# Kernel optimization log

Measured on AMD Instinct MI355X. Metric: run time of the kernel, lower is better.

Reference implementation:

```python
import jax, jax.numpy as jnp
import numpy as np

EPS = 1e-5  # BatchNorm eps


def _conv3x3(x, w, b):
    # x: [B,C,H,W], w: [O,C,3,3], b: [O]
    y = jax.lax.conv_general_dilated(
        x, w, window_strides=(1, 1), padding=((1, 1), (1, 1)),
        dimension_numbers=("NCHW", "OIHW", "NCHW"))
    return y + b[None, :, None, None]


def _bilinear_gather(x, py, px):
    """Bilinear sample x at fractional coords (zero outside bounds).
    x: [B,C,H,W]; py, px: [B,K,H,W] -> returns [B,C,K,H,W]."""
    B, C, H, W = x.shape
    K = py.shape[1]
    x_flat = x.reshape(B, C, H * W)
    y0 = jnp.floor(py)
    x0 = jnp.floor(px)
    wy1 = py - y0
    wx1 = px - x0
    wy0 = 1.0 - wy1
    wx0 = 1.0 - wx1

    def gather(yi, xi):
        valid = (yi >= 0) & (yi <= H - 1) & (xi >= 0) & (xi <= W - 1)
        yc = jnp.clip(yi, 0, H - 1).astype(jnp.int32)
        xc = jnp.clip(xi, 0, W - 1).astype(jnp.int32)
        idx = (yc * W + xc).reshape(B, 1, K * H * W)
        g = jnp.take_along_axis(x_flat, idx, axis=2).reshape(B, C, K, H, W)
        return g * valid.astype(x.dtype)[:, None]

    val = (gather(y0, x0) * (wy0 * wx0)[:, None]
           + gather(y0, x0 + 1.0) * (wy0 * wx1)[:, None]
           + gather(y0 + 1.0, x0) * (wy1 * wx0)[:, None]
           + gather(y0 + 1.0, x0 + 1.0) * (wy1 * wx1)[:, None])
    return val


def _deform_conv_bn_relu(x, w_off, b_off, w_dcn, b_dcn, gamma, beta):
    B, Ci, H, W = x.shape
    Co = w_dcn.shape[0]
    # offset/mask branch: 27 = 9 dy | 9 dx (cat, then interpreted interleaved) | 9 mask
    om = _conv3x3(x, w_off, b_off)                       # [B,27,H,W]
    offset = jnp.concatenate([om[:, :9], om[:, 9:18]], axis=1)  # [B,18,H,W]
    mask = jax.nn.sigmoid(om[:, 18:27])                  # [B,9,H,W]
    dy = offset[:, 0::2]                                 # [B,9,H,W]
    dx = offset[:, 1::2]                                 # [B,9,H,W]
    # base sampling grid: stride 1, pad 1, dilation 1, 3x3 kernel
    ky = jnp.repeat(jnp.arange(3, dtype=x.dtype), 3)     # [9]
    kx = jnp.tile(jnp.arange(3, dtype=x.dtype), 3)       # [9]
    hh = jnp.arange(H, dtype=x.dtype)
    ww = jnp.arange(W, dtype=x.dtype)
    py = dy + (hh - 1.0)[None, None, :, None] + ky[None, :, None, None]
    px = dx + (ww - 1.0)[None, None, None, :] + kx[None, :, None, None]
    sampled = _bilinear_gather(x, py, px)                # [B,Ci,9,H,W]
    sampled = sampled * mask[:, None]                    # modulated (DCNv2)
    out = jnp.einsum('bckhw,ock->bohw', sampled, w_dcn.reshape(Co, Ci, 9))
    out = out + b_dcn[None, :, None, None]
    # BatchNorm2d (training mode: batch statistics, biased variance) + ReLU
    mean = jnp.mean(out, axis=(0, 2, 3), keepdims=True)
    var = jnp.mean(jnp.square(out - mean), axis=(0, 2, 3), keepdims=True)
    bn = (out - mean) * jax.lax.rsqrt(var + EPS)
    bn = bn * gamma[None, :, None, None] + beta[None, :, None, None]
    return jax.nn.relu(bn)


def setup_inputs() -> dict:
    key = jax.random.key(0)
    k0, k1, k2 = jax.random.split(key, 3)
    B, Ci, Co, H, W = 2, 256, 256, 96, 96
    x = jax.random.normal(k0, (B, Ci, H, W), jnp.float32)
    # small offset-conv weights -> offsets within a few pixels (realistic after training)
    w_off = jax.random.normal(k1, (27, Ci, 3, 3), jnp.float32) * 0.01
    b_off = jnp.zeros((27,), jnp.float32)
    w_dcn = jax.random.normal(k2, (Co, Ci, 3, 3), jnp.float32) * (1.0 / np.sqrt(Ci * 9))
    b_dcn = jnp.zeros((Co,), jnp.float32)
    gamma = jnp.ones((Co,), jnp.float32)
    beta = jnp.zeros((Co,), jnp.float32)
    return {"x": x, "w_off": w_off, "b_off": b_off, "w_dcn": w_dcn,
            "b_dcn": b_dcn, "gamma": gamma, "beta": beta}


def reference(x, w_off, b_off, w_dcn, b_dcn, gamma, beta):
    return _deform_conv_bn_relu(x, w_off, b_off, w_dcn, b_dcn, gamma, beta)
```

## Files before the change

kernel.cpp:

```cpp
#include <hip/hip_runtime.h>


typedef unsigned short ushort_t;
typedef unsigned int uint_t;
typedef __attribute__((ext_vector_type(8))) short bf16x8;
typedef __attribute__((ext_vector_type(4))) float f32x4;
typedef __attribute__((ext_vector_type(2), aligned(4))) float f32x2a;
typedef __attribute__((ext_vector_type(2))) float f32x2v;

#define HH 96
#define WW 96
#define HWSZ 9216
#define CI 256
#define CO 256
#define NB 2
#define NPIX 18432
#define KTOT 2304

__device__ __forceinline__ ushort_t f2bf(float f) {
  unsigned int u = __float_as_uint(f);
  u += 0x7fffu + ((u >> 16) & 1u);
  return (ushort_t)(u >> 16);
}
__device__ __forceinline__ float u2f(uint_t u) { return __uint_as_float(u); }

__device__ __forceinline__ void gload16(const void* g, void* l) {
  __builtin_amdgcn_global_load_lds(
      (const __attribute__((address_space(1))) unsigned int*)g,
      (__attribute__((address_space(3))) unsigned int*)l, 16, 0, 0);
}

__global__ void cvt_w9(const float* __restrict__ w, ushort_t* __restrict__ o) {
  int i = blockIdx.x * 256 + threadIdx.x;
  int oo = i / KTOT;
  int kk = i - oo * KTOT;
  o[(kk >> 3) * 2048 + oo * 8 + (kk & 7)] = f2bf(w[i]);
}

__global__ void cvt_woff9(const float* __restrict__ w, ushort_t* __restrict__ o) {
  int i = blockIdx.x * 256 + threadIdx.x;
  int m = i / KTOT;
  int kk = i - m * KTOT;
  float v = (m < 27) ? w[m * KTOT + kk] : 0.f;
  o[(kk >> 3) * 256 + m * 8 + (kk & 7)] = f2bf(v);
}

__global__ __launch_bounds__(512, 2) void off_gemm(
    const float* __restrict__ x, const ushort_t* __restrict__ w27r,
    float* __restrict__ om_part) {
  __shared__ __align__(16) ushort_t A27[2][2048];
  __shared__ __align__(16) ushort_t B64[4096];
  __shared__ uint2 tbl[9][64];

  const int tid = threadIdx.x;
  const int lane = tid & 63, wid = tid >> 6;
  const int p0 = blockIdx.x * 64;
  const int part = blockIdx.y;
  const int bimg = p0 / HWSZ;
  const int hw0 = p0 - bimg * HWSZ;
  const float* xb = x + (size_t)bimg * CI * HWSZ;

  for (int e = tid; e < 576; e += 512) {
    int k = e >> 6, px = e & 63;
    int hw = hw0 + px, h = hw / WW, w_ = hw - h * WW;
    int dy = k / 3 - 1, dx = k % 3 - 1;
    bool ok = (h + dy >= 0) && (h + dy < HH) && (w_ + dx >= 0) && (w_ + dx < WW);
    tbl[k][px] = make_uint2(ok ? (uint_t)(hw + dy * WW + dx) : 0u,
                            ok ? 0x3f800000u : 0u);
  }

  const int lg = lane >> 4, lm = lane & 15;
  const int wr = wid >> 2, wc = wid & 3;
  f32x4 acc = (f32x4){0.f, 0.f, 0.f, 0.f};

  int cj[8], kj[8];
#pragma unroll
  for (int j = 0; j < 8; ++j) {
    int kk = part * 1152 + wid * 8 + j;
    cj[j] = kk / 9;
    kj[j] = kk - 9 * cj[j];
  }
  __syncthreads();

  float rv0[8], rm0[8], rv1[8], rm1[8];
  const int k0 = part * 18;

#define OG_RAW(RV, RM)                                                        \
  { _Pragma("unroll") for (int j = 0; j < 8; ++j) {                           \
      uint2 e_ = tbl[kj[j]][lane];                                            \
      RV[j] = xb[cj[j] * HWSZ + (int)e_.x];                                   \
      RM[j] = u2f(e_.y);                                                      \
      kj[j] += 1; cj[j] += 7;                                                 \
      if (kj[j] == 9) { kj[j] = 0; cj[j] += 1; } } }
#define OG_GA(CH, BUF)                                                        \
  gload16(w27r + (size_t)(CH) * 2048 + (tid & 255) * 8, &A27[BUF][(wid & 3) * 512]);
#define OG_STEP(CUR, RVC, RMC, RVN, RMN, KO)                                  \
  {                                                                           \
    if ((KO) < 17) {                                                          \
      OG_RAW(RVN, RMN)                                                        \
      OG_GA(k0 + (KO) + 1, (CUR) ^ 1)                                         \
      asm volatile("s_waitcnt vmcnt(10)" ::: "memory");                       \
    } else {                                                                  \
      asm volatile("s_waitcnt vmcnt(1)" ::: "memory");                        \
    }                                                                         \
    __builtin_amdgcn_sched_barrier(0);                                        \
    {                                                                         \
      ushort_t sv_[8] __attribute__((aligned(16)));                           \
      _Pragma("unroll") for (int j = 0; j < 8; ++j)                           \
        sv_[j] = f2bf(RVC[j] * RMC[j]);                                       \
      *(uint4*)&B64[tid * 8] = *(const uint4*)sv_;                            \
    }                                                                         \
    if ((KO) < 17) asm volatile("s_waitcnt vmcnt(9) lgkmcnt(0)" ::: "memory"); \
    else           asm volatile("s_waitcnt vmcnt(0) lgkmcnt(0)" ::: "memory"); \
    __builtin_amdgcn_s_barrier();                                             \
    __builtin_amdgcn_sched_barrier(0);                                        \
    _Pragma("unroll") for (int s = 0; s < 2; ++s) {                           \
      bf16x8 af = *(const bf16x8*)&A27[CUR][((s * 4 + lg) * 32 + wr * 16 + lm) * 8]; \
      bf16x8 bfv = *(const bf16x8*)&B64[((s * 4 + lg) * 64 + wc * 16 + lm) * 8];     \
      acc = __builtin_amdgcn_mfma_f32_16x16x32_bf16(af, bfv, acc, 0, 0, 0);   \
    }                                                                         \
    asm volatile("s_waitcnt lgkmcnt(0)" ::: "memory");                        \
    __builtin_amdgcn_s_barrier();                                             \
    __builtin_amdgcn_sched_barrier(0);                                        \
  }

  OG_RAW(rv0, rm0)
  OG_GA(k0, 0)
  for (int ko2 = 0; ko2 < 9; ++ko2) {
    const int ko = ko2 * 2;
    OG_STEP(0, rv0, rm0, rv1, rm1, ko)
    OG_STEP(1, rv1, rm1, rv0, rm0, ko + 1)
  }
#undef OG_RAW
#undef OG_GA
#undef OG_STEP

  int row = wr * 16 + lg * 4;
  int col = p0 + wc * 16 + lm;
#pragma unroll
  for (int r = 0; r < 4; ++r)
    if (row + r < 27)
      om_part[((size_t)(part * 27 + row + r)) * NPIX + col] = acc[r];
}

__global__ void prep_kernel(const float* __restrict__ om_part, const float* __restrict__ b_off,
                            uint_t* __restrict__ offs, float4* __restrict__ wts) {
  int n = blockIdx.x * 128 + threadIdx.x;
  float omv[27];
#pragma unroll
  for (int ch = 0; ch < 27; ++ch)
    omv[ch] = b_off[ch] + om_part[(size_t)ch * NPIX + n] +
              om_part[((size_t)(27 + ch)) * NPIX + n];
  int hw = n % HWSZ;
  int h = hw / WW, w = hw - h * WW;
#pragma unroll
  for (int k = 0; k < 9; ++k) {
    float dy = omv[2 * k], dx = omv[2 * k + 1];
    float mk = 1.f / (1.f + __expf(-omv[18 + k]));
    float py = dy + (float)(h - 1 + k / 3);
    float px = dx + (float)(w - 1 + k % 3);
    float y0f = floorf(py), x0f = floorf(px);
    int y0 = (int)y0f, x0 = (int)x0f;
    float wy1 = py - y0f, wx1 = px - x0f;
    float wy0 = 1.f - wy1, wx0 = 1.f - wx1;
    float vy0 = (y0 >= 0 && y0 <= HH - 1) ? 1.f : 0.f;
    float vy1 = (y0 + 1 >= 0 && y0 + 1 <= HH - 1) ? 1.f : 0.f;
    int yc0 = min(max(y0, 0), HH - 1), yc1 = min(max(y0 + 1, 0), HH - 1);
    int xa = min(max(x0, 0), WW - 2);
    float a_, b_;
    if (x0 >= 0 && x0 <= WW - 2)      { a_ = wx0; b_ = wx1; }
    else if (x0 == -1)                { a_ = wx1; b_ = 0.f; }
    else if (x0 == WW - 1)            { a_ = 0.f; b_ = wx0; }
    else                              { a_ = 0.f; b_ = 0.f; }
    float s0 = mk * vy0 * wy0, s1 = mk * vy1 * wy1;
    offs[(size_t)k * NPIX + n] = (uint_t)(yc0 * WW + xa) | ((uint_t)(yc1 * WW + xa) << 16);
    wts[(size_t)k * NPIX + n] = make_float4(a_ * s0, b_ * s0, a_ * s1, b_ * s1);
  }
}

__global__ __launch_bounds__(512, 2) void sample_lds(
    const float* __restrict__ x, const uint_t* __restrict__ offs,
    const float4* __restrict__ wts, ushort_t* __restrict__ S_g) {
  __shared__ __align__(16) float xl2[HWSZ * 2];
  const int tid = threadIdx.x;
  const int img = blockIdx.x >> 1;
  const int half = blockIdx.x & 1;
  const int cp = blockIdx.y;
  const int n0 = img * HWSZ + half * 4608;

  {
    const float* s0 = x + ((size_t)(img * CI + 2 * cp)) * HWSZ;
    const float* s1 = s0 + HWSZ;
#pragma unroll
    for (int i = 0; i < 9; ++i) {
      int col = i * 1024 + tid * 2;
      f32x2v c0 = *(const f32x2v*)(s0 + col);
      f32x2v c1 = *(const f32x2v*)(s1 + col);
      *(float4*)&xl2[col * 2] = make_float4(c0[0], c1[0], c0[1], c1[1]);
    }
  }
  __syncthreads();

  for (int j = 0; j < 9; ++j) {
    const int n = n0 + tid + j * 512;
    uint_t ofr[9]; float4 wtr[9];
#pragma unroll
    for (int k = 0; k < 9; ++k) {
      ofr[k] = offs[(size_t)k * NPIX + n];
      wtr[k] = wts[(size_t)k * NPIX + n];
    }
    uint_t pkw[9];
#pragma unroll
    for (int i = 0; i < 9; ++i) pkw[i] = 0u;
#pragma unroll
    for (int k = 0; k < 9; ++k) {
      const int o0 = (int)(ofr[k] & 0xffffu);
      const int o1 = (int)(ofr[k] >> 16);
      f32x2v pa0 = *(const f32x2v*)&xl2[o0 * 2];
      f32x2v pa1 = *(const f32x2v*)&xl2[o0 * 2 + 2];
      f32x2v pb0 = *(const f32x2v*)&xl2[o1 * 2];
      f32x2v pb1 = *(const f32x2v*)&xl2[o1 * 2 + 2];
      float v0 = wtr[k].x * pa0[0] + wtr[k].y * pa1[0] + wtr[k].z * pb0[0] + wtr[k].w * pb1[0];
      float v1 = wtr[k].x * pa0[1] + wtr[k].y * pa1[1] + wtr[k].z * pb0[1] + wtr[k].w * pb1[1];
      const int q0 = k, q1 = 9 + k;
      pkw[q0 >> 1] |= ((uint_t)f2bf(v0)) << ((q0 & 1) * 16);
      pkw[q1 >> 1] |= ((uint_t)f2bf(v1)) << ((q1 & 1) * 16);
    }
#pragma unroll
    for (int jj = 0; jj < 9; ++jj) {
      const int kk = cp * 18 + 2 * jj;
      *(uint_t*)&S_g[((size_t)(kk >> 3) * NPIX + n) * 8 + (kk & 7)] = pkw[jj];
    }
  }
}

__global__ __launch_bounds__(512, 2) void s_gemm(
    const ushort_t* __restrict__ w9r, const ushort_t* __restrict__ S_g,
    const float* __restrict__ b_dcn, float* __restrict__ out,
    float2* __restrict__ bnp2) {
  __shared__ __align__(16) ushort_t A[4][8192];
  __shared__ __align__(16) ushort_t S[4][2048];

  const int tid = threadIdx.x;
  const int lane = tid & 63, wid = tid >> 6;
  const int p0 = blockIdx.x * 64;
  const int bimg = p0 / HWSZ;
  const int hw0 = p0 - bimg * HWSZ;
  const int lg = lane >> 4, lm = lane & 15;
  const int wr = wid >> 1, wc = wid & 1;

  f32x4 acc[4][2];
#pragma unroll
  for (int i = 0; i < 4; ++i)
#pragma unroll
    for (int j = 0; j < 2; ++j) acc[i][j] = (f32x4){0.f, 0.f, 0.f, 0.f};

#define SG_STAGE(CH, BUF)                                                     \
  {                                                                           \
    gload16(w9r + (size_t)(CH) * 8192 + tid * 8, &A[BUF][wid * 512]);         \
    gload16(w9r + (size_t)(CH) * 8192 + 4096 + tid * 8, &A[BUF][4096 + wid * 512]); \
    if (wid < 4)                                                              \
      gload16(S_g + ((size_t)((CH) * 4 + wid) * NPIX + p0 + lane) * 8,        \
              &S[BUF][wid * 512]);                                            \
  }
#define SG_MFMA(BUF)                                                          \
  {                                                                           \
    bf16x8 bfr0 = *(const bf16x8*)&S[BUF][(lg * 64 + wc * 32 + lm) * 8];      \
    bf16x8 bfr1 = *(const bf16x8*)&S[BUF][(lg * 64 + wc * 32 + 16 + lm) * 8]; \
    _Pragma("unroll") for (int mi = 0; mi < 4; ++mi) {                        \
      bf16x8 af = *(const bf16x8*)&A[BUF][(lg * 256 + wr * 64 + mi * 16 + lm) * 8]; \
      acc[mi][0] = __builtin_amdgcn_mfma_f32_16x16x32_bf16(af, bfr0, acc[mi][0], 0, 0, 0); \
      acc[mi][1] = __builtin_amdgcn_mfma_f32_16x16x32_bf16(af, bfr1, acc[mi][1], 0, 0, 0); \
    }                                                                         \
  }

  SG_STAGE(0, 0)
  SG_STAGE(1, 1)
  for (int ko = 0; ko < 70; ++ko) {
    SG_STAGE(ko + 2, (ko + 2) & 3)
    if (wid < 4) { asm volatile("s_waitcnt vmcnt(6)" ::: "memory"); }
    else         { asm volatile("s_waitcnt vmcnt(4)" ::: "memory"); }
    __builtin_amdgcn_s_barrier();
    __builtin_amdgcn_sched_barrier(0);
    SG_MFMA(ko & 3)
  }
  if (wid < 4) { asm volatile("s_waitcnt vmcnt(3)" ::: "memory"); }
  else         { asm volatile("s_waitcnt vmcnt(2)" ::: "memory"); }
  __builtin_amdgcn_s_barrier();
  __builtin_amdgcn_sched_barrier(0);
  SG_MFMA(2)
  asm volatile("s_waitcnt vmcnt(0)" ::: "memory");
  __builtin_amdgcn_s_barrier();
  __builtin_amdgcn_sched_barrier(0);
  SG_MFMA(3)
#undef SG_STAGE
#undef SG_MFMA

  const int hwv0 = hw0 + wc * 32 + lm;
  float bsum[16], bsq[16];
#pragma unroll
  for (int mi = 0; mi < 4; ++mi) {
#pragma unroll
    for (int r = 0; r < 4; ++r) {
      int o = wr * 64 + mi * 16 + lg * 4 + r;
      float b = b_dcn[o];
      float v0 = acc[mi][0][r] + b;
      float v1 = acc[mi][1][r] + b;
      out[((size_t)(bimg * CO + o)) * HWSZ + hwv0] = v0;
      out[((size_t)(bimg * CO + o)) * HWSZ + hwv0 + 16] = v1;
      bsum[mi * 4 + r] = v0 + v1;
      bsq[mi * 4 + r] = v0 * v0 + v1 * v1;
    }
  }
#pragma unroll
  for (int d = 1; d < 16; d <<= 1) {
#pragma unroll
    for (int i = 0; i < 16; ++i) {
      bsum[i] += __shfl_xor(bsum[i], d);
      bsq[i] += __shfl_xor(bsq[i], d);
    }
  }
  asm volatile("s_waitcnt lgkmcnt(0)" ::: "memory");
  __builtin_amdgcn_s_barrier();
  float* red = (float*)&A[0][0];
  if (lm == 0) {
#pragma unroll
    for (int i = 0; i < 16; ++i) {
      int o = wr * 64 + (i >> 2) * 16 + lg * 4 + (i & 3);
      red[o * 2 + wc] = bsum[i];
      red[512 + o * 2 + wc] = bsq[i];
    }
  }
  __syncthreads();
  if (tid < 256) {
    float s = red[tid * 2] + red[tid * 2 + 1];
    float q = red[512 + tid * 2] + red[512 + tid * 2 + 1];
    bnp2[(size_t)tid * 288 + blockIdx.x] = make_float2(s, q);
  }
}

__global__ __launch_bounds__(256) void bn_finl(const float2* __restrict__ bnp2,
                                               const float* __restrict__ gamma,
                                               const float* __restrict__ beta,
                                               float* __restrict__ ss) {
  int o = threadIdx.x;
  float s = 0.f, q = 0.f;
  for (int j = 0; j < 288; ++j) {
    float2 p = bnp2[(size_t)o * 288 + j];
    s += p.x; q += p.y;
  }
  float mean = s * (1.f / (float)NPIX);
  float var = q * (1.f / (float)NPIX) - mean * mean;
  float rstd = rsqrtf(var + 1e-5f);
  float sc = rstd * gamma[o];
  ss[o] = sc;
  ss[CO + o] = beta[o] - mean * sc;
}

__global__ void bn_apply(float* __restrict__ out, const float* __restrict__ ss) {
  int i = blockIdx.x * 256 + threadIdx.x;
  float4 v = ((float4*)out)[i];
  int o = (i / (HWSZ / 4)) & 255;
  float sc = ss[o], sh = ss[CO + o];
  v.x = fmaxf(v.x * sc + sh, 0.f);
  v.y = fmaxf(v.y * sc + sh, 0.f);
  v.z = fmaxf(v.z * sc + sh, 0.f);
  v.w = fmaxf(v.w * sc + sh, 0.f);
  ((float4*)out)[i] = v;
}

extern "C" void kernel_launch(void* const* d_in, const int* in_sizes, int n_in,
                              void* d_out, int out_size, void* d_ws, size_t ws_size,
                              hipStream_t stream) {
  const float* x = (const float*)d_in[0];
  const float* w_off = (const float*)d_in[1];
  const float* b_off = (const float*)d_in[2];
  const float* w_dcn = (const float*)d_in[3];
  const float* b_dcn = (const float*)d_in[4];
  const float* gamma = (const float*)d_in[5];
  const float* beta = (const float*)d_in[6];
  float* out = (float*)d_out;

  char* ws = (char*)d_ws;

  size_t base = 84934656;
  ushort_t* S_g   = (ushort_t*)(ws);
  float*    om    = (float*)(ws + base);
  float2*   bnp2  = (float2*)(ws + base);
  uint_t*   offs  = (uint_t*)(ws + base + 3981312);
  float4*   wts   = (float4*)(ws + base + 4644864);
  ushort_t* w9r   = (ushort_t*)(ws + base + 7299072);
  ushort_t* w27r  = (ushort_t*)(ws + base + 8478720);
  float*    ss    = (float*)(ws + base + 8626176);

  cvt_w9<<<(CO * KTOT) / 256, 256, 0, stream>>>(w_dcn, w9r);
  cvt_woff9<<<(32 * KTOT) / 256, 256, 0, stream>>>(w_off, w27r);
  off_gemm<<<dim3(NPIX / 64, 2), 512, 0, stream>>>(x, w27r, om);
  prep_kernel<<<NPIX / 128, 128, 0, stream>>>(om, b_off, offs, wts);
  sample_lds<<<dim3(4, 128), 512, 0, stream>>>(x, offs, wts, S_g);
  s_gemm<<<NPIX / 64, 512, 0, stream>>>(w9r, S_g, b_dcn, out, bnp2);
  bn_finl<<<1, 256, 0, stream>>>(bnp2, gamma, beta, ss);
  bn_apply<<<(out_size / 4) / 256, 256, 0, stream>>>(out, ss);
}
```

Measured before the change: 161.2 us.

## Pack sampled input to bf16 in LDS, triple-buffer GEMM, parallelize BN finalize

The sampling kernel now stores the two-channel input tile in LDS as packed bf16 pairs instead of fp32. This halves LDS use, which may allow more resident blocks, and halves the bytes per gather, at the cost of rounding the input to bf16 before interpolation. The GEMM drops from a 4-deep to a 3-deep LDS ring and issues the prefetch after the barrier, trading load-latency slack for less shared memory. The BN finalize kernel goes from one block with a serial loop per channel to one 64-thread block per channel using a shuffle reduction.

```diff
diff --git a/kernel.cpp b/kernel.cpp
--- a/kernel.cpp
+++ b/kernel.cpp
@@ -181,7 +181,7 @@
 __global__ __launch_bounds__(512, 2) void sample_lds(
     const float* __restrict__ x, const uint_t* __restrict__ offs,
     const float4* __restrict__ wts, ushort_t* __restrict__ S_g) {
-  __shared__ __align__(16) float xl2[HWSZ * 2];
+  __shared__ __align__(8) uint_t xp[HWSZ];
   const int tid = threadIdx.x;
   const int img = blockIdx.x >> 1;
   const int half = blockIdx.x & 1;
@@ -196,7 +196,10 @@
       int col = i * 1024 + tid * 2;
       f32x2v c0 = *(const f32x2v*)(s0 + col);
       f32x2v c1 = *(const f32x2v*)(s1 + col);
-      *(float4*)&xl2[col * 2] = make_float4(c0[0], c1[0], c0[1], c1[1]);
+      uint2 pk;
+      pk.x = (uint_t)f2bf(c0[0]) | ((uint_t)f2bf(c1[0]) << 16);
+      pk.y = (uint_t)f2bf(c0[1]) | ((uint_t)f2bf(c1[1]) << 16);
+      *(uint2*)&xp[col] = pk;
     }
   }
   __syncthreads();
@@ -216,12 +219,12 @@
     for (int k = 0; k < 9; ++k) {
       const int o0 = (int)(ofr[k] & 0xffffu);
       const int o1 = (int)(ofr[k] >> 16);
-      f32x2v pa0 = *(const f32x2v*)&xl2[o0 * 2];
-      f32x2v pa1 = *(const f32x2v*)&xl2[o0 * 2 + 2];
-      f32x2v pb0 = *(const f32x2v*)&xl2[o1 * 2];
-      f32x2v pb1 = *(const f32x2v*)&xl2[o1 * 2 + 2];
-      float v0 = wtr[k].x * pa0[0] + wtr[k].y * pa1[0] + wtr[k].z * pb0[0] + wtr[k].w * pb1[0];
-      float v1 = wtr[k].x * pa0[1] + wtr[k].y * pa1[1] + wtr[k].z * pb0[1] + wtr[k].w * pb1[1];
+      uint_t a0 = xp[o0], a1 = xp[o0 + 1];
+      uint_t b0 = xp[o1], b1 = xp[o1 + 1];
+      float v0 = wtr[k].x * u2f(a0 << 16) + wtr[k].y * u2f(a1 << 16) +
+                 wtr[k].z * u2f(b0 << 16) + wtr[k].w * u2f(b1 << 16);
+      float v1 = wtr[k].x * u2f(a0 & 0xffff0000u) + wtr[k].y * u2f(a1 & 0xffff0000u) +
+                 wtr[k].z * u2f(b0 & 0xffff0000u) + wtr[k].w * u2f(b1 & 0xffff0000u);
       const int q0 = k, q1 = 9 + k;
       pkw[q0 >> 1] |= ((uint_t)f2bf(v0)) << ((q0 & 1) * 16);
       pkw[q1 >> 1] |= ((uint_t)f2bf(v1)) << ((q1 & 1) * 16);
@@ -238,8 +241,8 @@
     const ushort_t* __restrict__ w9r, const ushort_t* __restrict__ S_g,
     const float* __restrict__ b_dcn, float* __restrict__ out,
     float2* __restrict__ bnp2) {
-  __shared__ __align__(16) ushort_t A[4][8192];
-  __shared__ __align__(16) ushort_t S[4][2048];
+  __shared__ __align__(16) ushort_t A[3][8192];
+  __shared__ __align__(16) ushort_t S[3][2048];
 
   const int tid = threadIdx.x;
   const int lane = tid & 63, wid = tid >> 6;
@@ -276,23 +279,23 @@
 
   SG_STAGE(0, 0)
   SG_STAGE(1, 1)
-  for (int ko = 0; ko < 70; ++ko) {
-    SG_STAGE(ko + 2, (ko + 2) & 3)
-    if (wid < 4) { asm volatile("s_waitcnt vmcnt(6)" ::: "memory"); }
-    else         { asm volatile("s_waitcnt vmcnt(4)" ::: "memory"); }
-    __builtin_amdgcn_s_barrier();
-    __builtin_amdgcn_sched_barrier(0);
-    SG_MFMA(ko & 3)
-  }
-  if (wid < 4) { asm volatile("s_waitcnt vmcnt(3)" ::: "memory"); }
-  else         { asm volatile("s_waitcnt vmcnt(2)" ::: "memory"); }
-  __builtin_amdgcn_s_barrier();
-  __builtin_amdgcn_sched_barrier(0);
-  SG_MFMA(2)
-  asm volatile("s_waitcnt vmcnt(0)" ::: "memory");
-  __builtin_amdgcn_s_barrier();
-  __builtin_amdgcn_sched_barrier(0);
-  SG_MFMA(3)
+  {
+    int cur = 0, wrt = 2;
+    for (int ko = 0; ko < 72; ++ko) {
+      if (ko < 71) {
+        if (wid < 4) { asm volatile("s_waitcnt vmcnt(3)" ::: "memory"); }
+        else         { asm volatile("s_waitcnt vmcnt(2)" ::: "memory"); }
+      } else {
+        asm volatile("s_waitcnt vmcnt(0)" ::: "memory");
+      }
+      __builtin_amdgcn_s_barrier();
+      __builtin_amdgcn_sched_barrier(0);
+      if (ko < 70) SG_STAGE(ko + 2, wrt)
+      SG_MFMA(cur)
+      cur = (cur == 2) ? 0 : cur + 1;
+      wrt = (wrt == 2) ? 0 : wrt + 1;
+    }
+  }
 #undef SG_STAGE
 #undef SG_MFMA
 
@@ -339,22 +342,29 @@
   }
 }
 
-__global__ __launch_bounds__(256) void bn_finl(const float2* __restrict__ bnp2,
-                                               const float* __restrict__ gamma,
-                                               const float* __restrict__ beta,
-                                               float* __restrict__ ss) {
-  int o = threadIdx.x;
+__global__ __launch_bounds__(64) void bn_finl(const float2* __restrict__ bnp2,
+                                              const float* __restrict__ gamma,
+                                              const float* __restrict__ beta,
+                                              float* __restrict__ ss) {
+  int o = blockIdx.x, t = threadIdx.x;
   float s = 0.f, q = 0.f;
-  for (int j = 0; j < 288; ++j) {
+  for (int j = t; j < 288; j += 64) {
     float2 p = bnp2[(size_t)o * 288 + j];
     s += p.x; q += p.y;
   }
-  float mean = s * (1.f / (float)NPIX);
-  float var = q * (1.f / (float)NPIX) - mean * mean;
-  float rstd = rsqrtf(var + 1e-5f);
-  float sc = rstd * gamma[o];
-  ss[o] = sc;
-  ss[CO + o] = beta[o] - mean * sc;
+#pragma unroll
+  for (int d = 32; d > 0; d >>= 1) {
+    s += __shfl_xor(s, d);
+    q += __shfl_xor(q, d);
+  }
+  if (t == 0) {
+    float mean = s * (1.f / (float)NPIX);
+    float var = q * (1.f / (float)NPIX) - mean * mean;
+    float rstd = rsqrtf(var + 1e-5f);
+    float sc = rstd * gamma[o];
+    ss[o] = sc;
+    ss[CO + o] = beta[o] - mean * sc;
+  }
 }
 
 __global__ void bn_apply(float* __restrict__ out, const float* __restrict__ ss) {
@@ -399,6 +409,6 @@
   prep_kernel<<<NPIX / 128, 128, 0, stream>>>(om, b_off, offs, wts);
   sample_lds<<<dim3(4, 128), 512, 0, stream>>>(x, offs, wts, S_g);
   s_gemm<<<NPIX / 64, 512, 0, stream>>>(w9r, S_g, b_dcn, out, bnp2);
-  bn_finl<<<1, 256, 0, stream>>>(bnp2, gamma, beta, ss);
+  bn_finl<<<CO, 64, 0, stream>>>(bnp2, gamma, beta, ss);
   bn_apply<<<(out_size / 4) / 256, 256, 0, stream>>>(out, ss);
 }
```

New measurement: 160.4 us. No clear change (-0.5%).
